# Optimization experiments

Measured on AMD Instinct MI355X. Metric: run time of the kernel, lower is better.

## Reference

```python
import jax, jax.numpy as jnp
import numpy as np

B, N, C, H = 64, 4096, 128, 4
ALPHA = 0.2  # leaky_relu negative slope


def setup_inputs() -> dict:
    key = jax.random.key(0)
    k1, k2, k3, k4, k5 = jax.random.split(key, 5)
    V = jax.random.normal(k1, (B, N, C), dtype=jnp.float32)
    graph_size = jax.random.randint(k2, (B,), 1, N + 1, dtype=jnp.int32)
    # xavier_uniform-like init for weight [C, H*C] and tune_weight [1, H, C]
    lim_w = float(np.sqrt(6.0 / (C + H * C)))
    weight = jax.random.uniform(k3, (C, H * C), minval=-lim_w, maxval=lim_w, dtype=jnp.float32)
    lim_t = float(np.sqrt(6.0 / (H + C)))
    tune_weight = jax.random.uniform(k4, (1, H, C), minval=-lim_t, maxval=lim_t, dtype=jnp.float32)
    bias = jnp.full((H * C,), 0.01, dtype=jnp.float32)
    return {"V": V, "graph_size": graph_size, "weight": weight, "bias": bias, "tune_weight": tune_weight}


def reference(V, graph_size, weight, bias, tune_weight):
    # valid-node mask: node n of graph b is valid iff n < graph_size[b]
    mask = jnp.arange(N)[None, :] < graph_size[:, None]          # [B, N]
    # linear projection: [B, N, C] @ [C, H*C] + bias -> [B, N, H, C]
    Vg = (jnp.einsum('bnc,cd->bnd', V, weight) + bias).reshape(B, N, H, C)
    # attention logits per head: sum over features of tune_weight * Vg
    a = jnp.einsum('bnhc,ohc->bnh', Vg, tune_weight)             # [B, N, H]
    a = jnp.where(a >= 0, a, ALPHA * a)                          # leaky_relu
    # per-graph (segment) softmax over valid nodes
    a = jnp.where(mask[:, :, None], a, -jnp.inf)
    a = jax.nn.softmax(a, axis=1)                                # [B, N, H]
    # weighted segment sum -> [B, H, C] -> [B, H*C] (concat=True)
    out = jnp.einsum('bnhc,bnh->bhc', Vg, a)
    return out.reshape(B, H * C)
```

## Files before the change

kernel.cpp:

```cpp
#include <hip/hip_runtime.h>

#define NB 64
#define NN 4096
#define NC 128
#define NH 4
#define HC (NH * NC)
#define PSTRIDE (8 + HC)
#define NSLICE 16
#define LRELU 0.2f

__global__ __launch_bounds__(128) void k0_wt(const float* __restrict__ W,
                                             const float* __restrict__ bias,
                                             const float* __restrict__ tune,
                                             float* __restrict__ wtbt)
{
    const int bid = blockIdx.x;
    const int t = threadIdx.x;
    const float* src = (bid < NC) ? (W + (size_t)bid * HC) : bias;
    float* dst = (bid < NC) ? (wtbt + bid * NH) : (wtbt + NC * NH);
    const float4 a = reinterpret_cast<const float4*>(src)[t];
    const float4 b = reinterpret_cast<const float4*>(tune)[t];
    float p = a.x * b.x + a.y * b.y + a.z * b.z + a.w * b.w;
    #pragma unroll
    for (int off = 16; off; off >>= 1) p += __shfl_xor(p, off, 32);
    if ((t & 31) == 0) dst[t >> 5] = p;
}

__global__ __launch_bounds__(256, 4) void k1_part(const float* __restrict__ V,
                                                  const int* __restrict__ gs,
                                                  const float* __restrict__ wtbt,
                                                  float* __restrict__ part)
{
    const int slice = blockIdx.x;
    const int b = blockIdx.y;
    const int tid = threadIdx.x;
    const int hw = tid >> 5;
    const int lane = tid & 31;
    const int h = lane >> 3;
    const int j = lane & 7;
    const int w = slice * 8 + hw;
    const int gsz = gs[b];

    float wtk[16];
    #pragma unroll
    for (int u = 0; u < 16; ++u) wtk[u] = wtbt[(16 * j + u) * NH + h];
    const float bt = wtbt[HC + h];

    const int seg = (gsz + 127) >> 7;
    const int beg = w * seg;
    int iters = gsz - beg;
    iters = (iters < 0) ? 0 : (iters > seg ? seg : iters);

    float l = 0.f;
    float S[16] = {};

    const float* vp = V + ((size_t)b * NN + beg) * NC + j * 16;

    float4 A0, A1, A2, A3, B0, B1, B2, B3;
    if (iters > 0) {
        A0 = reinterpret_cast<const float4*>(vp)[0];
        A1 = reinterpret_cast<const float4*>(vp)[1];
        A2 = reinterpret_cast<const float4*>(vp)[2];
        A3 = reinterpret_cast<const float4*>(vp)[3];
        const float* p1 = vp + (iters > 1 ? NC : 0);
        B0 = reinterpret_cast<const float4*>(p1)[0];
        B1 = reinterpret_cast<const float4*>(p1)[1];
        B2 = reinterpret_cast<const float4*>(p1)[2];
        B3 = reinterpret_cast<const float4*>(p1)[3];
    }
    for (int i = 0; i < iters; ++i) {
        const float* p2 = vp + (i + 2 < iters ? 2 * NC : 0);
        const float4 C0 = reinterpret_cast<const float4*>(p2)[0];
        const float4 C1 = reinterpret_cast<const float4*>(p2)[1];
        const float4 C2 = reinterpret_cast<const float4*>(p2)[2];
        const float4 C3 = reinterpret_cast<const float4*>(p2)[3];
        vp += NC;

        float a0 = A0.x * wtk[0]  + A0.y * wtk[1]  + A0.z * wtk[2]  + A0.w * wtk[3];
        float a1 = A1.x * wtk[4]  + A1.y * wtk[5]  + A1.z * wtk[6]  + A1.w * wtk[7];
        float a2 = A2.x * wtk[8]  + A2.y * wtk[9]  + A2.z * wtk[10] + A2.w * wtk[11];
        float a3 = A3.x * wtk[12] + A3.y * wtk[13] + A3.z * wtk[14] + A3.w * wtk[15];
        float lg = (a0 + a1) + (a2 + a3);
        lg += __shfl_xor(lg, 1, 32);
        lg += __shfl_xor(lg, 2, 32);
        lg += __shfl_xor(lg, 4, 32);
        float x = lg + bt;
        x = (x >= 0.f) ? x : LRELU * x;
        const float p = __expf(x);
        l += p;
        S[0]  += p * A0.x;  S[1]  += p * A0.y;  S[2]  += p * A0.z;  S[3]  += p * A0.w;
        S[4]  += p * A1.x;  S[5]  += p * A1.y;  S[6]  += p * A1.z;  S[7]  += p * A1.w;
        S[8]  += p * A2.x;  S[9]  += p * A2.y;  S[10] += p * A2.z;  S[11] += p * A2.w;
        S[12] += p * A3.x;  S[13] += p * A3.y;  S[14] += p * A3.z;  S[15] += p * A3.w;
        A0 = B0; A1 = B1; A2 = B2; A3 = B3;
        B0 = C0; B1 = C1; B2 = C2; B3 = C3;
    }

    __shared__ float llds[8][4];
    __shared__ float Sall[8][4][132];
    if (j == 0) llds[hw][h] = l;
    #pragma unroll
    for (int t = 0; t < 4; ++t) {
        float4 s4;
        s4.x = S[4 * t]; s4.y = S[4 * t + 1]; s4.z = S[4 * t + 2]; s4.w = S[4 * t + 3];
        *reinterpret_cast<float4*>(&Sall[hw][h][16 * j + 4 * t]) = s4;
    }
    __syncthreads();
    float* pb = part + (size_t)(b * NSLICE + slice) * PSTRIDE;
    if (tid < 4) {
        float L = 0.f;
        #pragma unroll
        for (int ww = 0; ww < 8; ++ww) L += llds[ww][tid];
        pb[4 + tid] = L;
    }
    #pragma unroll
    for (int r = 0; r < 2; ++r) {
        const int e = tid + r * 256;
        const int hh = e >> 7, k = e & 127;
        float s = 0.f;
        #pragma unroll
        for (int ww = 0; ww < 8; ++ww) s += Sall[ww][hh][k];
        pb[8 + e] = s;
    }
}

__global__ __launch_bounds__(128) void k2_out(const float* __restrict__ part,
                                              const float* __restrict__ W,
                                              const float* __restrict__ bias,
                                              float* __restrict__ out)
{
    const int b = blockIdx.x;
    const int h = blockIdx.y;
    const int tid = threadIdx.x;
    const float* pb = part + (size_t)b * NSLICE * PSTRIDE;

    __shared__ float Sn[NC];
    __shared__ float sL;
    if (tid == 0) {
        float L = 0.f;
        #pragma unroll
        for (int c = 0; c < NSLICE; ++c) L += pb[(size_t)c * PSTRIDE + 4 + h];
        sL = L;
    }
    __syncthreads();
    {
        float s = 0.f;
        #pragma unroll 4
        for (int c = 0; c < NSLICE; ++c)
            s += pb[(size_t)c * PSTRIDE + 8 + h * NC + tid];
        Sn[tid] = s / sL;
    }
    __syncthreads();
    const int d = h * NC + tid;
    float acc = 0.f;
    #pragma unroll 4
    for (int k = 0; k < NC; ++k) acc += Sn[k] * W[(size_t)k * HC + d];
    out[(size_t)b * HC + d] = acc + bias[d];
}

extern "C" void kernel_launch(void* const* d_in, const int* in_sizes, int n_in,
                              void* d_out, int out_size, void* d_ws, size_t ws_size,
                              hipStream_t stream)
{
    const float* V    = (const float*)d_in[0];
    const int*   gsz  = (const int*)d_in[1];
    const float* W    = (const float*)d_in[2];
    const float* bias = (const float*)d_in[3];
    const float* tune = (const float*)d_in[4];
    float* out  = (float*)d_out;
    float* wtbt = (float*)d_ws;
    float* part = wtbt + PSTRIDE;

    hipLaunchKernelGGL(k0_wt, dim3(NC + 1), dim3(128), 0, stream, W, bias, tune, wtbt);
    hipLaunchKernelGGL(k1_part, dim3(NSLICE, NB), dim3(256), 0, stream, V, gsz, wtbt, part);
    hipLaunchKernelGGL(k2_out, dim3(NB, NH), dim3(128), 0, stream, part, W, bias, out);
}
```

Before: 51.26 us.

## Fuse weight precompute, segment softmax and output GEMV into one per-graph kernel

Replaces the three-kernel pipeline with a single kernel that runs one 1024-thread block per graph. Each block recomputes the tune-weight projection of W and bias into shared memory, streams its graph's nodes across 32 half-waves, reduces partial softmax sums in LDS, and then does the output GEMV split over two halves of K. The goal is to remove two launches and the global round-trip of partial sums. In exchange the grid shrinks to 64 blocks, so the V stream runs on far fewer CUs, graphs of unequal size load-balance poorly, and every block re-reads all of W for the precompute.

```diff
diff --git a/kernel.cpp b/kernel.cpp
--- a/kernel.cpp
+++ b/kernel.cpp
@@ -5,49 +5,68 @@
 #define NC 128
 #define NH 4
 #define HC (NH * NC)
-#define PSTRIDE (8 + HC)
-#define NSLICE 16
+#define NHW 32
 #define LRELU 0.2f
 
-__global__ __launch_bounds__(128) void k0_wt(const float* __restrict__ W,
-                                             const float* __restrict__ bias,
-                                             const float* __restrict__ tune,
-                                             float* __restrict__ wtbt)
+__global__ __launch_bounds__(1024, 4) void mega(const float* __restrict__ V,
+                                                const int* __restrict__ gs,
+                                                const float* __restrict__ W,
+                                                const float* __restrict__ bias,
+                                                const float* __restrict__ tune,
+                                                float* __restrict__ out)
 {
-    const int bid = blockIdx.x;
-    const int t = threadIdx.x;
-    const float* src = (bid < NC) ? (W + (size_t)bid * HC) : bias;
-    float* dst = (bid < NC) ? (wtbt + bid * NH) : (wtbt + NC * NH);
-    const float4 a = reinterpret_cast<const float4*>(src)[t];
-    const float4 b = reinterpret_cast<const float4*>(tune)[t];
-    float p = a.x * b.x + a.y * b.y + a.z * b.z + a.w * b.w;
-    #pragma unroll
-    for (int off = 16; off; off >>= 1) p += __shfl_xor(p, off, 32);
-    if ((t & 31) == 0) dst[t >> 5] = p;
-}
+    const int b = blockIdx.x;
+    const int tid = threadIdx.x;
 
-__global__ __launch_bounds__(256, 4) void k1_part(const float* __restrict__ V,
-                                                  const int* __restrict__ gs,
-                                                  const float* __restrict__ wtbt,
-                                                  float* __restrict__ part)
-{
-    const int slice = blockIdx.x;
-    const int b = blockIdx.y;
-    const int tid = threadIdx.x;
-    const int hw = tid >> 5;
+    __shared__ float tuneS[HC];
+    __shared__ float wtL[NC * NH];
+    __shared__ float btL[NH];
+    __shared__ float llds[NHW][NH];
+    __shared__ float Sall[NHW][NH][NC + 4];
+    __shared__ float LhS[NH];
+    __shared__ float SnS[NH][NC];
+    __shared__ float gemv[2][HC];
+
+    if (tid < HC / 4)
+        reinterpret_cast<float4*>(tuneS)[tid] = reinterpret_cast<const float4*>(tune)[tid];
+    __syncthreads();
+    if (tid < 512) {
+        const int k = tid >> 2, h = tid & 3;
+        const float* wrow = W + (size_t)k * HC + h * NC;
+        const float* trow = tuneS + h * NC;
+        float acc = 0.f;
+        #pragma unroll 8
+        for (int u = 0; u < NC / 4; ++u) {
+            const float4 wv = reinterpret_cast<const float4*>(wrow)[u];
+            const float4 tv = reinterpret_cast<const float4*>(trow)[u];
+            acc += wv.x * tv.x + wv.y * tv.y + wv.z * tv.z + wv.w * tv.w;
+        }
+        wtL[k * NH + h] = acc;
+    } else if (tid < 512 + 128) {
+        const int t2 = tid - 512;
+        const int h = t2 >> 5, l5 = t2 & 31;
+        const float4 bv = reinterpret_cast<const float4*>(bias + h * NC)[l5];
+        const float4 tv = reinterpret_cast<const float4*>(tuneS + h * NC)[l5];
+        float p = bv.x * tv.x + bv.y * tv.y + bv.z * tv.z + bv.w * tv.w;
+        #pragma unroll
+        for (int off = 16; off; off >>= 1) p += __shfl_xor(p, off, 32);
+        if (l5 == 0) btL[h] = p;
+    }
+    __syncthreads();
+
+    const int gsz = gs[b];
+    const int s = tid >> 5;
     const int lane = tid & 31;
     const int h = lane >> 3;
     const int j = lane & 7;
-    const int w = slice * 8 + hw;
-    const int gsz = gs[b];
 
     float wtk[16];
     #pragma unroll
-    for (int u = 0; u < 16; ++u) wtk[u] = wtbt[(16 * j + u) * NH + h];
-    const float bt = wtbt[HC + h];
+    for (int u = 0; u < 16; ++u) wtk[u] = wtL[(16 * j + u) * NH + h];
+    const float bt = btL[h];
 
-    const int seg = (gsz + 127) >> 7;
-    const int beg = w * seg;
+    const int seg = (gsz + NHW - 1) >> 5;
+    const int beg = s * seg;
     int iters = gsz - beg;
     iters = (iters < 0) ? 0 : (iters > seg ? seg : iters);
 
@@ -96,66 +115,43 @@
         B0 = C0; B1 = C1; B2 = C2; B3 = C3;
     }
 
-    __shared__ float llds[8][4];
-    __shared__ float Sall[8][4][132];
-    if (j == 0) llds[hw][h] = l;
+    if (j == 0) llds[s][h] = l;
     #pragma unroll
     for (int t = 0; t < 4; ++t) {
         float4 s4;
         s4.x = S[4 * t]; s4.y = S[4 * t + 1]; s4.z = S[4 * t + 2]; s4.w = S[4 * t + 3];
-        *reinterpret_cast<float4*>(&Sall[hw][h][16 * j + 4 * t]) = s4;
+        *reinterpret_cast<float4*>(&Sall[s][h][16 * j + 4 * t]) = s4;
     }
     __syncthreads();
-    float* pb = part + (size_t)(b * NSLICE + slice) * PSTRIDE;
-    if (tid < 4) {
+    if (tid < NH) {
         float L = 0.f;
         #pragma unroll
-        for (int ww = 0; ww < 8; ++ww) L += llds[ww][tid];
-        pb[4 + tid] = L;
+        for (int ss = 0; ss < NHW; ++ss) L += llds[ss][tid];
+        LhS[tid] = L;
     }
-    #pragma unroll
-    for (int r = 0; r < 2; ++r) {
-        const int e = tid + r * 256;
-        const int hh = e >> 7, k = e & 127;
-        float s = 0.f;
+    __syncthreads();
+    if (tid < 512) {
+        const int hh = tid >> 7, k = tid & 127;
+        float ssum = 0.f;
         #pragma unroll
-        for (int ww = 0; ww < 8; ++ww) s += Sall[ww][hh][k];
-        pb[8 + e] = s;
-    }
-}
-
-__global__ __launch_bounds__(128) void k2_out(const float* __restrict__ part,
-                                              const float* __restrict__ W,
-                                              const float* __restrict__ bias,
-                                              float* __restrict__ out)
-{
-    const int b = blockIdx.x;
-    const int h = blockIdx.y;
-    const int tid = threadIdx.x;
-    const float* pb = part + (size_t)b * NSLICE * PSTRIDE;
-
-    __shared__ float Sn[NC];
-    __shared__ float sL;
-    if (tid == 0) {
-        float L = 0.f;
-        #pragma unroll
-        for (int c = 0; c < NSLICE; ++c) L += pb[(size_t)c * PSTRIDE + 4 + h];
-        sL = L;
+        for (int ss = 0; ss < NHW; ++ss) ssum += Sall[ss][hh][k];
+        SnS[hh][k] = ssum / LhS[hh];
     }
     __syncthreads();
     {
-        float s = 0.f;
-        #pragma unroll 4
-        for (int c = 0; c < NSLICE; ++c)
-            s += pb[(size_t)c * PSTRIDE + 8 + h * NC + tid];
-        Sn[tid] = s / sL;
+        const int d = tid & 511;
+        const int halfk = tid >> 9;
+        const int hh = d >> 7;
+        const float* wcol = W + (size_t)(halfk * 64) * HC + d;
+        const float* snp = &SnS[hh][halfk * 64];
+        float acc = 0.f;
+        #pragma unroll 8
+        for (int k = 0; k < 64; ++k) acc += snp[k] * wcol[(size_t)k * HC];
+        gemv[halfk][d] = acc;
     }
     __syncthreads();
-    const int d = h * NC + tid;
-    float acc = 0.f;
-    #pragma unroll 4
-    for (int k = 0; k < NC; ++k) acc += Sn[k] * W[(size_t)k * HC + d];
-    out[(size_t)b * HC + d] = acc + bias[d];
+    if (tid < 512)
+        out[(size_t)b * HC + tid] = gemv[0][tid] + gemv[1][tid] + bias[tid];
 }
 
 extern "C" void kernel_launch(void* const* d_in, const int* in_sizes, int n_in,
@@ -167,11 +163,7 @@
     const float* W    = (const float*)d_in[2];
     const float* bias = (const float*)d_in[3];
     const float* tune = (const float*)d_in[4];
-    float* out  = (float*)d_out;
-    float* wtbt = (float*)d_ws;
-    float* part = wtbt + PSTRIDE;
+    float* out = (float*)d_out;
 
-    hipLaunchKernelGGL(k0_wt, dim3(NC + 1), dim3(128), 0, stream, W, bias, tune, wtbt);
-    hipLaunchKernelGGL(k1_part, dim3(NSLICE, NB), dim3(256), 0, stream, V, gsz, wtbt, part);
-    hipLaunchKernelGGL(k2_out, dim3(NB, NH), dim3(128), 0, stream, part, W, bias, out);
+    hipLaunchKernelGGL(mega, dim3(NB), dim3(1024), 0, stream, V, gsz, W, bias, tune, out);
 }
```

After: 124.7 us. 2.43x slower.

## Stage V tiles through shared memory with coalesced block-wide loads

Applied to the files above, without the earlier changes.

Replaces the per-half-warp strided streaming of V rows with cooperative, fully coalesced loads of 64-row tiles into LDS. Each half-warp then reads 8 rows from shared memory to compute logits and weighted sums. Rows are now partitioned per slice and masked by a validity flag. The aim is better global-memory coalescing, at the cost of two barriers per tile, losing the register prefetch pipelining, and 32KB of LDS, which may lower occupancy.

```diff
diff --git a/kernel.cpp b/kernel.cpp
--- a/kernel.cpp
+++ b/kernel.cpp
@@ -7,6 +7,7 @@
 #define HC (NH * NC)
 #define PSTRIDE (8 + HC)
 #define NSLICE 16
+#define TROWS 64
 #define LRELU 0.2f
 
 __global__ __launch_bounds__(128) void k0_wt(const float* __restrict__ W,
@@ -31,6 +32,11 @@
                                                   const float* __restrict__ wtbt,
                                                   float* __restrict__ part)
 {
+    __shared__ float smem[8192];
+    float (*Vt)[NC] = reinterpret_cast<float(*)[NC]>(smem);
+    float (*Sall)[NH][132] = reinterpret_cast<float(*)[NH][132]>(smem);
+    float* llds = smem + 8 * NH * 132;
+
     const int slice = blockIdx.x;
     const int b = blockIdx.y;
     const int tid = threadIdx.x;
@@ -38,7 +44,6 @@
     const int lane = tid & 31;
     const int h = lane >> 3;
     const int j = lane & 7;
-    const int w = slice * 8 + hw;
     const int gsz = gs[b];
 
     float wtk[16];
@@ -46,59 +51,67 @@
     for (int u = 0; u < 16; ++u) wtk[u] = wtbt[(16 * j + u) * NH + h];
     const float bt = wtbt[HC + h];
 
-    const int seg = (gsz + 127) >> 7;
-    const int beg = w * seg;
-    int iters = gsz - beg;
-    iters = (iters < 0) ? 0 : (iters > seg ? seg : iters);
+    const int segB = (gsz + NSLICE - 1) / NSLICE;
+    const int myBeg = slice * segB;
+    int myEnd = myBeg + segB;
+    if (myEnd > gsz) myEnd = gsz;
+    const int nrows = (myEnd > myBeg) ? (myEnd - myBeg) : 0;
+    const int ntile = (nrows + TROWS - 1) / TROWS;
 
     float l = 0.f;
     float S[16] = {};
 
-    const float* vp = V + ((size_t)b * NN + beg) * NC + j * 16;
+    const float4* Vg4 = reinterpret_cast<const float4*>(V);
+    const size_t gbase = (size_t)b * NN;
 
-    float4 A0, A1, A2, A3, B0, B1, B2, B3;
-    if (iters > 0) {
-        A0 = reinterpret_cast<const float4*>(vp)[0];
-        A1 = reinterpret_cast<const float4*>(vp)[1];
-        A2 = reinterpret_cast<const float4*>(vp)[2];
-        A3 = reinterpret_cast<const float4*>(vp)[3];
-        const float* p1 = vp + (iters > 1 ? NC : 0);
-        B0 = reinterpret_cast<const float4*>(p1)[0];
-        B1 = reinterpret_cast<const float4*>(p1)[1];
-        B2 = reinterpret_cast<const float4*>(p1)[2];
-        B3 = reinterpret_cast<const float4*>(p1)[3];
-    }
-    for (int i = 0; i < iters; ++i) {
-        const float* p2 = vp + (i + 2 < iters ? 2 * NC : 0);
-        const float4 C0 = reinterpret_cast<const float4*>(p2)[0];
-        const float4 C1 = reinterpret_cast<const float4*>(p2)[1];
-        const float4 C2 = reinterpret_cast<const float4*>(p2)[2];
-        const float4 C3 = reinterpret_cast<const float4*>(p2)[3];
-        vp += NC;
-
-        float a0 = A0.x * wtk[0]  + A0.y * wtk[1]  + A0.z * wtk[2]  + A0.w * wtk[3];
-        float a1 = A1.x * wtk[4]  + A1.y * wtk[5]  + A1.z * wtk[6]  + A1.w * wtk[7];
-        float a2 = A2.x * wtk[8]  + A2.y * wtk[9]  + A2.z * wtk[10] + A2.w * wtk[11];
-        float a3 = A3.x * wtk[12] + A3.y * wtk[13] + A3.z * wtk[14] + A3.w * wtk[15];
-        float lg = (a0 + a1) + (a2 + a3);
-        lg += __shfl_xor(lg, 1, 32);
-        lg += __shfl_xor(lg, 2, 32);
-        lg += __shfl_xor(lg, 4, 32);
-        float x = lg + bt;
-        x = (x >= 0.f) ? x : LRELU * x;
-        const float p = __expf(x);
-        l += p;
-        S[0]  += p * A0.x;  S[1]  += p * A0.y;  S[2]  += p * A0.z;  S[3]  += p * A0.w;
-        S[4]  += p * A1.x;  S[5]  += p * A1.y;  S[6]  += p * A1.z;  S[7]  += p * A1.w;
-        S[8]  += p * A2.x;  S[9]  += p * A2.y;  S[10] += p * A2.z;  S[11] += p * A2.w;
-        S[12] += p * A3.x;  S[13] += p * A3.y;  S[14] += p * A3.z;  S[15] += p * A3.w;
-        A0 = B0; A1 = B1; A2 = B2; A3 = B3;
-        B0 = C0; B1 = C1; B2 = C2; B3 = C3;
+    for (int tile = 0; tile < ntile; ++tile) {
+        const int tbase = myBeg + tile * TROWS;
+        float4 r[8];
+        #pragma unroll
+        for (int k = 0; k < 8; ++k) {
+            const int idx = tid + (k << 8);
+            const int row = idx >> 5;
+            const int gr = tbase + row;
+            const int src_row = (gr < myEnd) ? gr : myBeg;
+            r[k] = Vg4[(gbase + src_row) * 32 + (idx & 31)];
+        }
+        #pragma unroll
+        for (int k = 0; k < 8; ++k) {
+            const int idx = tid + (k << 8);
+            reinterpret_cast<float4*>(smem)[idx] = r[k];
+        }
+        __syncthreads();
+        #pragma unroll 2
+        for (int rr = 0; rr < 8; ++rr) {
+            const int row = (hw << 3) + rr;
+            const bool valid = (tbase + row < myEnd);
+            const float4* vr = reinterpret_cast<const float4*>(&Vt[row][j * 16]);
+            const float4 A0 = vr[0];
+            const float4 A1 = vr[1];
+            const float4 A2 = vr[2];
+            const float4 A3 = vr[3];
+            float a0 = A0.x * wtk[0]  + A0.y * wtk[1]  + A0.z * wtk[2]  + A0.w * wtk[3];
+            float a1 = A1.x * wtk[4]  + A1.y * wtk[5]  + A1.z * wtk[6]  + A1.w * wtk[7];
+            float a2 = A2.x * wtk[8]  + A2.y * wtk[9]  + A2.z * wtk[10] + A2.w * wtk[11];
+            float a3 = A3.x * wtk[12] + A3.y * wtk[13] + A3.z * wtk[14] + A3.w * wtk[15];
+            float lg = (a0 + a1) + (a2 + a3);
+            lg += __shfl_xor(lg, 1, 32);
+            lg += __shfl_xor(lg, 2, 32);
+            lg += __shfl_xor(lg, 4, 32);
+            float x = lg + bt;
+            x = (x >= 0.f) ? x : LRELU * x;
+            float p = __expf(x);
+            p = valid ? p : 0.f;
+            l += p;
+            S[0]  += p * A0.x;  S[1]  += p * A0.y;  S[2]  += p * A0.z;  S[3]  += p * A0.w;
+            S[4]  += p * A1.x;  S[5]  += p * A1.y;  S[6]  += p * A1.z;  S[7]  += p * A1.w;
+            S[8]  += p * A2.x;  S[9]  += p * A2.y;  S[10] += p * A2.z;  S[11] += p * A2.w;
+            S[12] += p * A3.x;  S[13] += p * A3.y;  S[14] += p * A3.z;  S[15] += p * A3.w;
+        }
+        __syncthreads();
     }
 
-    __shared__ float llds[8][4];
-    __shared__ float Sall[8][4][132];
-    if (j == 0) llds[hw][h] = l;
+    if (j == 0) llds[hw * NH + h] = l;
     #pragma unroll
     for (int t = 0; t < 4; ++t) {
         float4 s4;
@@ -110,12 +123,12 @@
     if (tid < 4) {
         float L = 0.f;
         #pragma unroll
-        for (int ww = 0; ww < 8; ++ww) L += llds[ww][tid];
+        for (int ww = 0; ww < 8; ++ww) L += llds[ww * NH + tid];
         pb[4 + tid] = L;
     }
     #pragma unroll
-    for (int r = 0; r < 2; ++r) {
-        const int e = tid + r * 256;
+    for (int r2 = 0; r2 < 2; ++r2) {
+        const int e = tid + r2 * 256;
         const int hh = e >> 7, k = e & 127;
         float s = 0.f;
         #pragma unroll
```

After: 44.20 us. 1.16x faster.
